# Kernel tuning notes

Measured on AMD Instinct MI355X. Metric: run time of the kernel, lower is better.

The kernel has to match this reference:

```python
import jax, jax.numpy as jnp
import numpy as np

N = 50000      # nodes
IN = 128       # in_channels
H = 2          # heads
C = 64         # hidden_channels (per head)
E = 800000     # edges (before self-loops)
OUT = 40       # out_channels
BN_EPS = 1e-5
NEG_SLOPE = 0.2  # PyG GATConv default


def _bn(x, g, b):
    # BatchNorm1d forward with batch statistics (training-mode math, biased var)
    mu = jnp.mean(x, axis=0)
    v = jnp.var(x, axis=0)
    return (x - mu) * jax.lax.rsqrt(v + BN_EPS) * g + b


def _gat_conv(x, src, dst, W, a_src, a_dst, bias, concat):
    n = x.shape[0]
    h = (x @ W).reshape(n, H, C)                      # [N,H,C] per-head projection
    al_s = jnp.einsum('nhc,hc->nh', h, a_src)         # [N,H]
    al_d = jnp.einsum('nhc,hc->nh', h, a_dst)
    e = jax.nn.leaky_relu(al_s[src] + al_d[dst], NEG_SLOPE)  # [E,H]
    # segment softmax over edges sharing the same destination
    m = jax.ops.segment_max(e, dst, num_segments=n)
    ex = jnp.exp(e - m[dst])
    s = jax.ops.segment_sum(ex, dst, num_segments=n)
    alpha = ex / s[dst]                               # [E,H]
    out = jax.ops.segment_sum(h[src] * alpha[..., None], dst, num_segments=n)  # [N,H,C]
    out = out.reshape(n, H * C) if concat else out.mean(axis=1)
    return out + bias


def setup_inputs() -> dict:
    key = jax.random.key(0)
    ks = jax.random.split(key, 16)
    g = lambda k, shp, scale=1.0: jax.random.normal(k, shp, dtype=jnp.float32) * scale
    x = g(ks[0], (N, IN))
    edge_index = jax.random.randint(ks[1], (2, E), 0, N, dtype=jnp.int32)
    s = 1.0 / np.sqrt(IN)
    s2 = 1.0 / np.sqrt(H * C)
    return {
        'x': x,
        'edge_index': edge_index,
        'bn0_g': jnp.ones((IN,), jnp.float32), 'bn0_b': jnp.zeros((IN,), jnp.float32),
        'W1': g(ks[2], (IN, H * C), s), 'a1_src': g(ks[3], (H, C), s), 'a1_dst': g(ks[4], (H, C), s),
        'b1': jnp.zeros((H * C,), jnp.float32),
        'bn1_g': jnp.ones((H * C,), jnp.float32), 'bn1_b': jnp.zeros((H * C,), jnp.float32),
        'W2': g(ks[5], (H * C, H * C), s2), 'a2_src': g(ks[6], (H, C), s2), 'a2_dst': g(ks[7], (H, C), s2),
        'b2': jnp.zeros((C,), jnp.float32),
        'bn2_g': jnp.ones((C,), jnp.float32), 'bn2_b': jnp.zeros((C,), jnp.float32),
        'Wf': g(ks[8], (C, OUT), 1.0 / np.sqrt(C)), 'bf': jnp.zeros((OUT,), jnp.float32),
    }


def reference(x, edge_index, bn0_g, bn0_b, W1, a1_src, a1_dst, b1, bn1_g, bn1_b,
              W2, a2_src, a2_dst, b2, bn2_g, bn2_b, Wf, bf):
    n = x.shape[0]
    loop = jnp.arange(n, dtype=edge_index.dtype)
    src = jnp.concatenate([edge_index[0], loop])  # add self-loops (PyG default)
    dst = jnp.concatenate([edge_index[1], loop])
    h = _bn(x, bn0_g, bn0_b)
    # layer 1: concat heads
    h = _gat_conv(h, src, dst, W1, a1_src, a1_dst, b1, concat=True)
    h = jax.nn.elu(_bn(h, bn1_g, bn1_b))
    # (dropout is identity in eval mode)
    # layer 2: average heads
    h = _gat_conv(h, src, dst, W2, a2_src, a2_dst, b2, concat=False)
    h = jax.nn.elu(_bn(h, bn2_g, bn2_b))
    return h @ Wf + bf
```

## Files before the change

kernel.cpp:

```cpp
#include <hip/hip_runtime.h>
#include <hip/hip_fp16.h>


#define NEG_SLOPE 0.2f
#define BN_EPS 1e-5f

typedef short bf16x8 __attribute__((ext_vector_type(8)));
typedef float f32x4 __attribute__((ext_vector_type(4)));

static __device__ __forceinline__ unsigned short f2bf(float f) {
    union { float f; unsigned u; } v; v.f = f;
    unsigned r = v.u + 0x7FFF + ((v.u >> 16) & 1);
    return (unsigned short)(r >> 16);
}
static __device__ __forceinline__ float2 bf2x2(unsigned v) {
    union { unsigned u; float f; } a, b;
    a.u = v << 16; b.u = v & 0xffff0000u;
    return make_float2(a.f, b.f);
}
static __device__ __forceinline__ float halfsel(unsigned p, int head) {
    __half2 h = *(__half2*)&p;
    return head ? __high2float(h) : __low2float(h);
}

__global__ void k_rank(const int* __restrict__ ei, int E, int Nn,
                       int* __restrict__ cnt, int* __restrict__ rank) {
    int i = blockIdx.x * blockDim.x + threadIdx.x;
    if (i >= E + Nn) return;
    int d = (i < E) ? ei[E + i] : (i - E);
    rank[i] = atomicAdd(&cnt[d], 1);
}

__global__ __launch_bounds__(1024) void k_part(const int* __restrict__ cnt, int Nn,
                                               int* __restrict__ part) {
    __shared__ int ws[16];
    int t = threadIdx.x, lane = t & 63, w = t >> 6;
    int i = blockIdx.x * 1024 + t;
    int v = (i < Nn) ? cnt[i] : 0;
    #pragma unroll
    for (int off = 32; off; off >>= 1) v += __shfl_xor(v, off);
    if (lane == 0) ws[w] = v;
    __syncthreads();
    if (t < 16) {
        int s = ws[t];
        #pragma unroll
        for (int off = 8; off; off >>= 1) s += __shfl_xor(s, off);
        if (t == 0) part[blockIdx.x] = s;
    }
}

__global__ __launch_bounds__(64) void k_scanp(int* __restrict__ part, int nb,
                                              int Nn, int* __restrict__ rowptr) {
    int lane = threadIdx.x;
    int carry = 0;
    for (int base = 0; base < nb; base += 64) {
        int i = base + lane;
        int v = (i < nb) ? part[i] : 0;
        int x = v;
        #pragma unroll
        for (int off = 1; off < 64; off <<= 1) {
            int y = __shfl_up(x, off);
            if (lane >= off) x += y;
        }
        if (i < nb) part[i] = carry + x - v;
        carry += __shfl(x, 63);
    }
    if (lane == 0) rowptr[Nn] = carry;
}

__global__ __launch_bounds__(1024) void k_scan2(const int* __restrict__ cnt, int Nn,
                                                const int* __restrict__ part,
                                                int* __restrict__ rowptr) {
    __shared__ int wsum[16];
    int t = threadIdx.x, lane = t & 63, w = t >> 6;
    int i = blockIdx.x * 1024 + t;
    int v = (i < Nn) ? cnt[i] : 0;
    int x = v;
    #pragma unroll
    for (int off = 1; off < 64; off <<= 1) {
        int y = __shfl_up(x, off);
        if (lane >= off) x += y;
    }
    if (lane == 63) wsum[w] = x;
    __syncthreads();
    if (w == 0) {
        int val = (lane < 16) ? wsum[lane] : 0;
        int xs = val;
        #pragma unroll
        for (int off = 1; off < 16; off <<= 1) {
            int y = __shfl_up(xs, off);
            if (lane >= off) xs += y;
        }
        if (lane < 16) wsum[lane] = xs - val;
    }
    __syncthreads();
    if (i < Nn) rowptr[i] = part[blockIdx.x] + wsum[w] + (x - v);
}

__global__ void k_fill2(const int* __restrict__ ei, const int* __restrict__ rank,
                        const int* __restrict__ rowptr, int E, int Nn,
                        int* __restrict__ ssrc) {
    int i = blockIdx.x * blockDim.x + threadIdx.x;
    if (i >= E + Nn) return;
    int s, d;
    if (i < E) { s = ei[i]; d = ei[E + i]; }
    else       { s = i - E; d = s; }
    ssrc[rowptr[d] + rank[i]] = s;
}

template <int C>
__global__ __launch_bounds__(256) void k_bnstat2(const float* __restrict__ x, int M,
                                                 int rowsPerBlock, float* __restrict__ sums) {
    constexpr int TPR = C / 4;
    constexpr int RS  = 256 / TPR;
    __shared__ float red[4][2 * C];
    const int t = threadIdx.x;
    const int cg = t % TPR, rg = t / TPR, w = t >> 6, lane = t & 63;
    int r0 = blockIdx.x * rowsPerBlock + rg;
    int r1 = min(M, blockIdx.x * rowsPerBlock + rowsPerBlock);
    float4 s = make_float4(0, 0, 0, 0), q = make_float4(0, 0, 0, 0);
    #pragma unroll 4
    for (int r = r0; r < r1; r += RS) {
        float4 v = *(const float4*)&x[(size_t)r * C + cg * 4];
        s.x += v.x; s.y += v.y; s.z += v.z; s.w += v.w;
        q.x += v.x * v.x; q.y += v.y * v.y; q.z += v.z * v.z; q.w += v.w * v.w;
    }
    #pragma unroll
    for (int off = TPR; off < 64; off <<= 1) {
        s.x += __shfl_xor(s.x, off); s.y += __shfl_xor(s.y, off);
        s.z += __shfl_xor(s.z, off); s.w += __shfl_xor(s.w, off);
        q.x += __shfl_xor(q.x, off); q.y += __shfl_xor(q.y, off);
        q.z += __shfl_xor(q.z, off); q.w += __shfl_xor(q.w, off);
    }
    if (lane < TPR) {
        *(float4*)&red[w][cg * 4] = s;
        *(float4*)&red[w][C + cg * 4] = q;
    }
    __syncthreads();
    for (int idx = t; idx < 2 * C; idx += 256) {
        float tot = red[0][idx] + red[1][idx] + red[2][idx] + red[3][idx];
        atomicAdd(&sums[idx], tot);
    }
}

__global__ void k_bnfin(const float* __restrict__ sums, int M, int C,
                        const float* __restrict__ g, const float* __restrict__ b,
                        float* __restrict__ st) {
    int c = threadIdx.x;
    if (c < C) {
        float mu = sums[c] / (float)M;
        float var = sums[C + c] / (float)M - mu * mu;
        float s = g[c] * rsqrtf(var + BN_EPS);
        st[c] = s;
        st[C + c] = b[c] - mu * s;
    }
}

__global__ __launch_bounds__(256) void k_wt2(const float* __restrict__ W1, const float* __restrict__ W2,
                                             unsigned short* __restrict__ wt1, unsigned short* __restrict__ wt2) {
    int idx = blockIdx.x * 256 + threadIdx.x;
    if (idx >= 128 * 128) return;
    int n = idx >> 7, k = idx & 127;
    wt1[idx] = f2bf(W1[k * 128 + n]);
    wt2[idx] = f2bf(W2[k * 128 + n]);
}

__global__ __launch_bounds__(256) void k_mfma(
    const float* __restrict__ A, const unsigned short* __restrict__ wt,
    const float* __restrict__ stp, int elu,
    const float* __restrict__ asrc, const float* __restrict__ adst, int M,
    unsigned short* __restrict__ hb, float* __restrict__ als, float* __restrict__ ald) {
    __shared__ unsigned short As[64 * 136];
    __shared__ unsigned short Bs[128 * 136];
    const int t = threadIdx.x;
    const int w = t >> 6, lane = t & 63;
    const int c = lane & 15, q = lane >> 4;
    const int row0 = blockIdx.x * 64;

    #pragma unroll
    for (int i = 0; i < 8; i++) {
        int idx = t + i * 256;
        int r = idx >> 5, ch4 = idx & 31;
        int gr = row0 + r;
        float4 v = make_float4(0, 0, 0, 0);
        if (gr < M) {
            v = *(const float4*)&A[(size_t)gr * 128 + ch4 * 4];
            float4 sc = *(const float4*)&stp[ch4 * 4];
            float4 sh = *(const float4*)&stp[128 + ch4 * 4];
            v.x = v.x * sc.x + sh.x; v.y = v.y * sc.y + sh.y;
            v.z = v.z * sc.z + sh.z; v.w = v.w * sc.w + sh.w;
            if (elu) {
                v.x = v.x > 0.f ? v.x : expm1f(v.x);
                v.y = v.y > 0.f ? v.y : expm1f(v.y);
                v.z = v.z > 0.f ? v.z : expm1f(v.z);
                v.w = v.w > 0.f ? v.w : expm1f(v.w);
            }
        }
        unsigned p0 = ((unsigned)f2bf(v.y) << 16) | f2bf(v.x);
        unsigned p1 = ((unsigned)f2bf(v.w) << 16) | f2bf(v.z);
        *(uint2*)&As[r * 136 + ch4 * 4] = make_uint2(p0, p1);
    }
    #pragma unroll
    for (int i = 0; i < 8; i++) {
        int idx = t + i * 256;
        int r = idx >> 4, ch = idx & 15;
        *(uint4*)&Bs[r * 136 + ch * 8] = *(const uint4*)&wt[(size_t)r * 128 + ch * 8];
    }
    __syncthreads();

    f32x4 acc[8] = {};
    #pragma unroll
    for (int ks = 0; ks < 4; ks++) {
        bf16x8 a = *(bf16x8*)&As[(w * 16 + c) * 136 + (ks * 4 + q) * 8];
        #pragma unroll
        for (int tl = 0; tl < 8; tl++) {
            bf16x8 b = *(bf16x8*)&Bs[(tl * 16 + c) * 136 + (ks * 4 + q) * 8];
            acc[tl] = __builtin_amdgcn_mfma_f32_16x16x32_bf16(a, b, acc[tl], 0, 0, 0);
        }
    }

    #pragma unroll
    for (int reg = 0; reg < 4; reg++) {
        int grow = row0 + w * 16 + q * 4 + reg;
        if (grow < M) {
            #pragma unroll
            for (int tl = 0; tl < 8; tl++)
                hb[(size_t)grow * 128 + tl * 16 + c] = f2bf(acc[tl][reg]);
        }
    }

    float as_[8], ad_[8];
    #pragma unroll
    for (int tl = 0; tl < 8; tl++) { as_[tl] = asrc[tl * 16 + c]; ad_[tl] = adst[tl * 16 + c]; }
    #pragma unroll
    for (int reg = 0; reg < 4; reg++) {
        float s0 = 0.f, s1 = 0.f, d0 = 0.f, d1 = 0.f;
        #pragma unroll
        for (int tl = 0; tl < 4; tl++) { s0 += acc[tl][reg] * as_[tl]; d0 += acc[tl][reg] * ad_[tl]; }
        #pragma unroll
        for (int tl = 4; tl < 8; tl++) { s1 += acc[tl][reg] * as_[tl]; d1 += acc[tl][reg] * ad_[tl]; }
        #pragma unroll
        for (int off = 1; off < 16; off <<= 1) {
            s0 += __shfl_xor(s0, off); s1 += __shfl_xor(s1, off);
            d0 += __shfl_xor(d0, off); d1 += __shfl_xor(d1, off);
        }
        int grow = row0 + w * 16 + q * 4 + reg;
        if (c == 0 && grow < M) {
            *(float2*)&als[(size_t)grow * 2] = make_float2(s0, s1);
            *(float2*)&ald[(size_t)grow * 2] = make_float2(d0, d1);
        }
    }
}

static __device__ __forceinline__ void acc8(float* acc, uint4 v, float a) {
    float2 p;
    p = bf2x2(v.x); acc[0] += a * p.x; acc[1] += a * p.y;
    p = bf2x2(v.y); acc[2] += a * p.x; acc[3] += a * p.y;
    p = bf2x2(v.z); acc[4] += a * p.x; acc[5] += a * p.y;
    p = bf2x2(v.w); acc[6] += a * p.x; acc[7] += a * p.y;
}

template <int MEAN>
static __device__ __forceinline__ void attnagg(
    const int* __restrict__ rowptr, const int* __restrict__ ssrc,
    const float* __restrict__ als, const float* __restrict__ ald,
    float* __restrict__ alpha, const unsigned short* __restrict__ hb,
    const float* __restrict__ bias, int Nn, float* __restrict__ out) {
    int gw = (blockIdx.x * blockDim.x + threadIdx.x) >> 6;
    if (gw >= Nn) return;
    int lane = threadIdx.x & 63;
    int sub = lane >> 4, c = lane & 15, head = c >> 3;
    int beg = rowptr[gw], end = rowptr[gw + 1];
    int deg = end - beg;
    float2 dv = *(const float2*)&ald[(size_t)gw * 2];
    float acc[8] = {};

    if (deg <= 64) {
        bool on = lane < deg;
        int eidx = beg + (on ? lane : 0);
        int sreg = ssrc[eidx];
        float2 av = *(const float2*)&als[(size_t)sreg * 2];
        float v0 = av.x + dv.x; v0 = v0 > 0.f ? v0 : NEG_SLOPE * v0;
        float v1 = av.y + dv.y; v1 = v1 > 0.f ? v1 : NEG_SLOPE * v1;
        float m0 = on ? v0 : -1e30f, m1 = on ? v1 : -1e30f;
        #pragma unroll
        for (int off = 32; off; off >>= 1) {
            m0 = fmaxf(m0, __shfl_xor(m0, off));
            m1 = fmaxf(m1, __shfl_xor(m1, off));
        }
        float p0 = on ? __expf(v0 - m0) : 0.f;
        float p1 = on ? __expf(v1 - m1) : 0.f;
        float t0 = p0, t1 = p1;
        #pragma unroll
        for (int off = 32; off; off >>= 1) {
            t0 += __shfl_xor(t0, off);
            t1 += __shfl_xor(t1, off);
        }
        __half2 hpk = __floats2half2_rn(p0 / t0, p1 / t1);
        int pk = *(int*)&hpk;

        int nit = (deg + 3) >> 2;
        for (int it = 0; it < nit; it += 2) {
            int j0 = it * 4 + sub;
            int j1 = j0 + 4;
            int sa = __shfl(sreg, j0 & 63);
            int sb = __shfl(sreg, j1 & 63);
            unsigned pa = (unsigned)__shfl(pk, j0 & 63);
            unsigned pb = (unsigned)__shfl(pk, j1 & 63);
            float aa = halfsel(pa, head);
            float ab = halfsel(pb, head);
            if (j0 < deg) {
                uint4 va = *(const uint4*)&hb[(size_t)sa * 128 + c * 8];
                acc8(acc, va, aa);
            }
            if (j1 < deg) {
                uint4 vb = *(const uint4*)&hb[(size_t)sb * 128 + c * 8];
                acc8(acc, vb, ab);
            }
        }
    } else {
        float d0 = dv.x, d1 = dv.y;
        float m0 = -1e30f, m1 = -1e30f;
        for (int e = beg + lane; e < end; e += 64) {
            int s = ssrc[e];
            float v0 = als[s * 2] + d0;     v0 = v0 > 0.f ? v0 : NEG_SLOPE * v0;
            float v1 = als[s * 2 + 1] + d1; v1 = v1 > 0.f ? v1 : NEG_SLOPE * v1;
            m0 = fmaxf(m0, v0); m1 = fmaxf(m1, v1);
        }
        #pragma unroll
        for (int off = 32; off; off >>= 1) {
            m0 = fmaxf(m0, __shfl_xor(m0, off));
            m1 = fmaxf(m1, __shfl_xor(m1, off));
        }
        float t0 = 0.f, t1 = 0.f;
        for (int e = beg + lane; e < end; e += 64) {
            int s = ssrc[e];
            float v0 = als[s * 2] + d0;     v0 = v0 > 0.f ? v0 : NEG_SLOPE * v0;
            float v1 = als[s * 2 + 1] + d1; v1 = v1 > 0.f ? v1 : NEG_SLOPE * v1;
            float p0 = __expf(v0 - m0), p1 = __expf(v1 - m1);
            alpha[e * 2] = p0; alpha[e * 2 + 1] = p1;
            t0 += p0; t1 += p1;
        }
        #pragma unroll
        for (int off = 32; off; off >>= 1) {
            t0 += __shfl_xor(t0, off);
            t1 += __shfl_xor(t1, off);
        }
        float i0 = 1.f / t0, i1 = 1.f / t1;
        for (int e = beg + sub; e < end; e += 4) {
            int s = ssrc[e];
            float a = (head ? alpha[(size_t)e * 2 + 1] * i1 : alpha[(size_t)e * 2] * i0);
            uint4 v = *(const uint4*)&hb[(size_t)s * 128 + c * 8];
            acc8(acc, v, a);
        }
    }

    #pragma unroll
    for (int j2 = 0; j2 < 8; j2++) {
        acc[j2] += __shfl_xor(acc[j2], 16);
        acc[j2] += __shfl_xor(acc[j2], 32);
        if (MEAN) acc[j2] += __shfl_xor(acc[j2], 8);
    }
    if (MEAN) {
        if (sub == 0 && c < 8) {
            float4 b0 = *(const float4*)&bias[c * 8];
            float4 b1 = *(const float4*)&bias[c * 8 + 4];
            float4 o0 = make_float4(0.5f * acc[0] + b0.x, 0.5f * acc[1] + b0.y, 0.5f * acc[2] + b0.z, 0.5f * acc[3] + b0.w);
            float4 o1 = make_float4(0.5f * acc[4] + b1.x, 0.5f * acc[5] + b1.y, 0.5f * acc[6] + b1.z, 0.5f * acc[7] + b1.w);
            *(float4*)&out[(size_t)gw * 64 + c * 8] = o0;
            *(float4*)&out[(size_t)gw * 64 + c * 8 + 4] = o1;
        }
    } else {
        if (sub == 0) {
            float4 b0 = *(const float4*)&bias[c * 8];
            float4 b1 = *(const float4*)&bias[c * 8 + 4];
            float4 o0 = make_float4(acc[0] + b0.x, acc[1] + b0.y, acc[2] + b0.z, acc[3] + b0.w);
            float4 o1 = make_float4(acc[4] + b1.x, acc[5] + b1.y, acc[6] + b1.z, acc[7] + b1.w);
            *(float4*)&out[(size_t)gw * 128 + c * 8] = o0;
            *(float4*)&out[(size_t)gw * 128 + c * 8 + 4] = o1;
        }
    }
}

__global__ __launch_bounds__(256) void k_attnagg1(const int* __restrict__ rowptr, const int* __restrict__ ssrc,
                                                  const float* __restrict__ als, const float* __restrict__ ald,
                                                  float* __restrict__ alpha, const unsigned short* __restrict__ hb,
                                                  const float* __restrict__ bias, int Nn, float* __restrict__ out) {
    attnagg<0>(rowptr, ssrc, als, ald, alpha, hb, bias, Nn, out);
}

__global__ __launch_bounds__(256) void k_attnagg2(const int* __restrict__ rowptr, const int* __restrict__ ssrc,
                                                  const float* __restrict__ als, const float* __restrict__ ald,
                                                  float* __restrict__ alpha, const unsigned short* __restrict__ hb,
                                                  const float* __restrict__ bias, int Nn, float* __restrict__ out) {
    attnagg<1>(rowptr, ssrc, als, ald, alpha, hb, bias, Nn, out);
}

__global__ __launch_bounds__(128) void k_gemmf(const float* __restrict__ A, const float* __restrict__ Wf,
                                               const float* __restrict__ bf, const float* __restrict__ st,
                                               int M, float* __restrict__ out) {
    __shared__ float As[128 * 65];
    __shared__ float Bs[64 * 40];
    int t = threadIdx.x;
    int row0 = blockIdx.x * 128;
    for (int i = t; i < 64 * 40; i += 128) Bs[i] = Wf[i];
    for (int i = t; i < 128 * 64; i += 128) {
        int r = i >> 6, k = i & 63;
        int gr = row0 + r;
        float v = 0.f;
        if (gr < M) {
            v = A[(size_t)gr * 64 + k] * st[k] + st[64 + k];
            v = v > 0.f ? v : expm1f(v);
        }
        As[r * 65 + k] = v;
    }
    __syncthreads();
    int cg = t & 3, rg = t >> 2;
    float acc[4][10] = {};
    for (int k = 0; k < 64; k++) {
        float b[10];
        #pragma unroll
        for (int j = 0; j < 10; j++) b[j] = Bs[k * 40 + cg * 10 + j];
        #pragma unroll
        for (int r = 0; r < 4; r++) {
            float a = As[(rg * 4 + r) * 65 + k];
            #pragma unroll
            for (int j = 0; j < 10; j++) acc[r][j] += a * b[j];
        }
    }
    for (int r = 0; r < 4; r++) {
        int gr = row0 + rg * 4 + r;
        if (gr < M) {
            #pragma unroll
            for (int j = 0; j < 10; j++) out[(size_t)gr * 40 + cg * 10 + j] = acc[r][j] + bf[cg * 10 + j];
        }
    }
}

extern "C" void kernel_launch(void* const* d_in, const int* in_sizes, int n_in,
                              void* d_out, int out_size, void* d_ws, size_t ws_size,
                              hipStream_t stream) {
    const float* x     = (const float*)d_in[0];
    const int*   ei    = (const int*)d_in[1];
    const float* bn0_g = (const float*)d_in[2];
    const float* bn0_b = (const float*)d_in[3];
    const float* W1    = (const float*)d_in[4];
    const float* a1s   = (const float*)d_in[5];
    const float* a1d   = (const float*)d_in[6];
    const float* b1    = (const float*)d_in[7];
    const float* bn1_g = (const float*)d_in[8];
    const float* bn1_b = (const float*)d_in[9];
    const float* W2    = (const float*)d_in[10];
    const float* a2s   = (const float*)d_in[11];
    const float* a2d   = (const float*)d_in[12];
    const float* b2    = (const float*)d_in[13];
    const float* bn2_g = (const float*)d_in[14];
    const float* bn2_b = (const float*)d_in[15];
    const float* Wf    = (const float*)d_in[16];
    const float* bf    = (const float*)d_in[17];
    float* out = (float*)d_out;

    const int N  = in_sizes[0] / 128;
    const int E  = in_sizes[1] / 2;
    const int ET = E + N;

    char* ws = (char*)d_ws;
    size_t off = 0;
    auto alloc = [&](size_t bytes) -> char* {
        char* p = ws + off;
        off = (off + bytes + 255) & ~(size_t)255;
        return p;
    };
    int*   cnt    = (int*)alloc((size_t)N * 4);
    int*   rowptr = (int*)alloc((size_t)(N + 1) * 4);
    int*   ssrc   = (int*)alloc((size_t)ET * 4);
    float* abuf   = (float*)alloc((size_t)N * 128 * 4);
    unsigned short* hb  = (unsigned short*)alloc((size_t)N * 128 * 2);
    unsigned short* wt1 = (unsigned short*)alloc((size_t)128 * 128 * 2);
    unsigned short* wt2 = (unsigned short*)alloc((size_t)128 * 128 * 2);
    float* alpha  = (float*)alloc((size_t)ET * 2 * 4);
    float* als    = (float*)alloc((size_t)N * 2 * 4);
    float* ald    = (float*)alloc((size_t)N * 2 * 4);
    int*   part   = (int*)alloc(1024 * 4);
    float* sums   = (float*)alloc(640 * 4);
    float* st     = (float*)alloc(256 * 4);
    int*   rank   = (int*)hb;

    const int tb = 256;
    const int egrid = (ET + tb - 1) / tb;
    const int wgrid = ((size_t)N * 64 + tb - 1) / tb;
    const int ggrid = (N + 63) / 64;
    const int nscan = (N + 1023) / 1024;
    const int bgrid = (N + 255) / 256;

    hipMemsetAsync(cnt, 0, (size_t)N * 4, stream);
    hipMemsetAsync(sums, 0, 640 * 4, stream);
    k_rank<<<egrid, tb, 0, stream>>>(ei, E, N, cnt, rank);
    k_part<<<nscan, 1024, 0, stream>>>(cnt, N, part);
    k_scanp<<<1, 64, 0, stream>>>(part, nscan, N, rowptr);
    k_scan2<<<nscan, 1024, 0, stream>>>(cnt, N, part, rowptr);
    k_fill2<<<egrid, tb, 0, stream>>>(ei, rank, rowptr, E, N, ssrc);

    k_wt2<<<64, tb, 0, stream>>>(W1, W2, wt1, wt2);

    k_bnstat2<128><<<bgrid, 256, 0, stream>>>(x, N, 256, sums);
    k_bnfin<<<1, 128, 0, stream>>>(sums, N, 128, bn0_g, bn0_b, st);

    k_mfma<<<ggrid, tb, 0, stream>>>(x, wt1, st, 0, a1s, a1d, N, hb, als, ald);
    k_attnagg1<<<wgrid, tb, 0, stream>>>(rowptr, ssrc, als, ald, alpha, hb, b1, N, abuf);

    k_bnstat2<128><<<bgrid, 256, 0, stream>>>(abuf, N, 256, sums + 256);
    k_bnfin<<<1, 128, 0, stream>>>(sums + 256, N, 128, bn1_g, bn1_b, st);

    k_mfma<<<ggrid, tb, 0, stream>>>(abuf, wt2, st, 1, a2s, a2d, N, hb, als, ald);
    k_attnagg2<<<wgrid, tb, 0, stream>>>(rowptr, ssrc, als, ald, alpha, hb, b2, N, abuf);

    k_bnstat2<64><<<bgrid, 256, 0, stream>>>(abuf, N, 256, sums + 512);
    k_bnfin<<<1, 64, 0, stream>>>(sums + 512, N, 64, bn2_g, bn2_b, st);

    k_gemmf<<<(N + 127) / 128, 128, 0, stream>>>(abuf, Wf, bf, st, N, out);
}
```

Measured before the change: 340.4 us.

## Fuse small setup kernels, use last-block BN finalize, unroll gather loop

Result: slower. 365.3 us (+7.3%).

```diff
diff --git a/kernel.cpp b/kernel.cpp
--- a/kernel.cpp
+++ b/kernel.cpp
@@ -23,12 +23,23 @@
     return head ? __high2float(h) : __low2float(h);
 }
 
-__global__ void k_rank(const int* __restrict__ ei, int E, int Nn,
-                       int* __restrict__ cnt, int* __restrict__ rank) {
+__global__ void k_rankwt(const int* __restrict__ ei, int E, int Nn, int egrid,
+                         int* __restrict__ cnt, unsigned short* __restrict__ rank,
+                         const float* __restrict__ W1, const float* __restrict__ W2,
+                         unsigned short* __restrict__ wt1, unsigned short* __restrict__ wt2) {
+    if (blockIdx.x >= egrid) {
+        int idx = (blockIdx.x - egrid) * 256 + threadIdx.x;
+        if (idx < 128 * 128) {
+            int n = idx >> 7, k = idx & 127;
+            wt1[idx] = f2bf(W1[k * 128 + n]);
+            wt2[idx] = f2bf(W2[k * 128 + n]);
+        }
+        return;
+    }
     int i = blockIdx.x * blockDim.x + threadIdx.x;
     if (i >= E + Nn) return;
     int d = (i < E) ? ei[E + i] : (i - E);
-    rank[i] = atomicAdd(&cnt[d], 1);
+    rank[i] = (unsigned short)atomicAdd(&cnt[d], 1);
 }
 
 __global__ __launch_bounds__(1024) void k_part(const int* __restrict__ cnt, int Nn,
@@ -49,31 +60,29 @@
     }
 }
 
-__global__ __launch_bounds__(64) void k_scanp(int* __restrict__ part, int nb,
-                                              int Nn, int* __restrict__ rowptr) {
-    int lane = threadIdx.x;
-    int carry = 0;
-    for (int base = 0; base < nb; base += 64) {
-        int i = base + lane;
-        int v = (i < nb) ? part[i] : 0;
-        int x = v;
-        #pragma unroll
-        for (int off = 1; off < 64; off <<= 1) {
-            int y = __shfl_up(x, off);
-            if (lane >= off) x += y;
-        }
-        if (i < nb) part[i] = carry + x - v;
-        carry += __shfl(x, 63);
-    }
-    if (lane == 0) rowptr[Nn] = carry;
-}
-
-__global__ __launch_bounds__(1024) void k_scan2(const int* __restrict__ cnt, int Nn,
+__global__ __launch_bounds__(1024) void k_scan2(const int* __restrict__ cnt, int Nn, int nb,
                                                 const int* __restrict__ part,
                                                 int* __restrict__ rowptr) {
     __shared__ int wsum[16];
+    __shared__ int s_base, s_total;
     int t = threadIdx.x, lane = t & 63, w = t >> 6;
-    int i = blockIdx.x * 1024 + t;
+    int b = blockIdx.x;
+    if (w == 0) {
+        int base = 0, total = 0;
+        for (int ch = 0; ch < nb; ch += 64) {
+            int j = ch + lane;
+            int v = (j < nb) ? part[j] : 0;
+            total += v;
+            base += (j < b) ? v : 0;
+        }
+        #pragma unroll
+        for (int off = 32; off; off >>= 1) {
+            base += __shfl_xor(base, off);
+            total += __shfl_xor(total, off);
+        }
+        if (lane == 0) { s_base = base; s_total = total; }
+    }
+    int i = b * 1024 + t;
     int v = (i < Nn) ? cnt[i] : 0;
     int x = v;
     #pragma unroll
@@ -94,10 +103,11 @@
         if (lane < 16) wsum[lane] = xs - val;
     }
     __syncthreads();
-    if (i < Nn) rowptr[i] = part[blockIdx.x] + wsum[w] + (x - v);
-}
-
-__global__ void k_fill2(const int* __restrict__ ei, const int* __restrict__ rank,
+    if (i < Nn) rowptr[i] = s_base + wsum[w] + (x - v);
+    if (b == gridDim.x - 1 && t == 0) rowptr[Nn] = s_total;
+}
+
+__global__ void k_fill2(const int* __restrict__ ei, const unsigned short* __restrict__ rank,
                         const int* __restrict__ rowptr, int E, int Nn,
                         int* __restrict__ ssrc) {
     int i = blockIdx.x * blockDim.x + threadIdx.x;
@@ -105,15 +115,18 @@
     int s, d;
     if (i < E) { s = ei[i]; d = ei[E + i]; }
     else       { s = i - E; d = s; }
-    ssrc[rowptr[d] + rank[i]] = s;
+    ssrc[rowptr[d] + (int)rank[i]] = s;
 }
 
 template <int C>
 __global__ __launch_bounds__(256) void k_bnstat2(const float* __restrict__ x, int M,
-                                                 int rowsPerBlock, float* __restrict__ sums) {
+                                                 int rowsPerBlock, float* __restrict__ sums,
+                                                 const float* __restrict__ g, const float* __restrict__ b,
+                                                 float* __restrict__ st, int* __restrict__ ticket) {
     constexpr int TPR = C / 4;
     constexpr int RS  = 256 / TPR;
     __shared__ float red[4][2 * C];
+    __shared__ int lastFlag;
     const int t = threadIdx.x;
     const int cg = t % TPR, rg = t / TPR, w = t >> 6, lane = t & 63;
     int r0 = blockIdx.x * rowsPerBlock + rg;
@@ -141,28 +154,21 @@
         float tot = red[0][idx] + red[1][idx] + red[2][idx] + red[3][idx];
         atomicAdd(&sums[idx], tot);
     }
-}
-
-__global__ void k_bnfin(const float* __restrict__ sums, int M, int C,
-                        const float* __restrict__ g, const float* __restrict__ b,
-                        float* __restrict__ st) {
-    int c = threadIdx.x;
-    if (c < C) {
-        float mu = sums[c] / (float)M;
-        float var = sums[C + c] / (float)M - mu * mu;
-        float s = g[c] * rsqrtf(var + BN_EPS);
-        st[c] = s;
-        st[C + c] = b[c] - mu * s;
-    }
-}
-
-__global__ __launch_bounds__(256) void k_wt2(const float* __restrict__ W1, const float* __restrict__ W2,
-                                             unsigned short* __restrict__ wt1, unsigned short* __restrict__ wt2) {
-    int idx = blockIdx.x * 256 + threadIdx.x;
-    if (idx >= 128 * 128) return;
-    int n = idx >> 7, k = idx & 127;
-    wt1[idx] = f2bf(W1[k * 128 + n]);
-    wt2[idx] = f2bf(W2[k * 128 + n]);
+    __threadfence();
+    if (t == 0) {
+        int old = __hip_atomic_fetch_add(ticket, 1, __ATOMIC_ACQ_REL, __HIP_MEMORY_SCOPE_AGENT);
+        lastFlag = (old == (int)gridDim.x - 1);
+    }
+    __syncthreads();
+    if (lastFlag && t < C) {
+        float ss = __hip_atomic_load(&sums[t], __ATOMIC_RELAXED, __HIP_MEMORY_SCOPE_AGENT);
+        float qq = __hip_atomic_load(&sums[C + t], __ATOMIC_RELAXED, __HIP_MEMORY_SCOPE_AGENT);
+        float mu = ss / (float)M;
+        float var = qq / (float)M - mu * mu;
+        float sc = g[t] * rsqrtf(var + BN_EPS);
+        st[t] = sc;
+        st[C + t] = b[t] - mu * sc;
+    }
 }
 
 __global__ __launch_bounds__(256) void k_mfma(
@@ -300,22 +306,21 @@
         int pk = *(int*)&hpk;
 
         int nit = (deg + 3) >> 2;
-        for (int it = 0; it < nit; it += 2) {
-            int j0 = it * 4 + sub;
-            int j1 = j0 + 4;
-            int sa = __shfl(sreg, j0 & 63);
-            int sb = __shfl(sreg, j1 & 63);
-            unsigned pa = (unsigned)__shfl(pk, j0 & 63);
-            unsigned pb = (unsigned)__shfl(pk, j1 & 63);
-            float aa = halfsel(pa, head);
-            float ab = halfsel(pb, head);
-            if (j0 < deg) {
-                uint4 va = *(const uint4*)&hb[(size_t)sa * 128 + c * 8];
-                acc8(acc, va, aa);
+        for (int it = 0; it < nit; it += 4) {
+            int jj[4], s_[4]; unsigned p_[4];
+            #pragma unroll
+            for (int u = 0; u < 4; u++) {
+                jj[u] = (it + u) * 4 + sub;
+                int ls = jj[u] & 63;
+                s_[u] = __shfl(sreg, ls);
+                p_[u] = (unsigned)__shfl(pk, ls);
             }
-            if (j1 < deg) {
-                uint4 vb = *(const uint4*)&hb[(size_t)sb * 128 + c * 8];
-                acc8(acc, vb, ab);
+            #pragma unroll
+            for (int u = 0; u < 4; u++) {
+                if (jj[u] < deg) {
+                    uint4 v = *(const uint4*)&hb[(size_t)s_[u] * 128 + c * 8];
+                    acc8(acc, v, halfsel(p_[u], head));
+                }
             }
         }
     } else {
@@ -482,9 +487,10 @@
     float* als    = (float*)alloc((size_t)N * 2 * 4);
     float* ald    = (float*)alloc((size_t)N * 2 * 4);
     int*   part   = (int*)alloc(1024 * 4);
-    float* sums   = (float*)alloc(640 * 4);
+    float* sums   = (float*)alloc(768 * 4);
     float* st     = (float*)alloc(256 * 4);
-    int*   rank   = (int*)hb;
+    unsigned short* rank = (unsigned short*)hb;
+    int* tickets = (int*)(sums + 640);
 
     const int tb = 256;
     const int egrid = (ET + tb - 1) / tb;
@@ -494,29 +500,23 @@
     const int bgrid = (N + 255) / 256;
 
     hipMemsetAsync(cnt, 0, (size_t)N * 4, stream);
-    hipMemsetAsync(sums, 0, 640 * 4, stream);
-    k_rank<<<egrid, tb, 0, stream>>>(ei, E, N, cnt, rank);
+    hipMemsetAsync(sums, 0, 768 * 4, stream);
+    k_rankwt<<<egrid + 64, tb, 0, stream>>>(ei, E, N, egrid, cnt, rank, W1, W2, wt1, wt2);
     k_part<<<nscan, 1024, 0, stream>>>(cnt, N, part);
-    k_scanp<<<1, 64, 0, stream>>>(part, nscan, N, rowptr);
-    k_scan2<<<nscan, 1024, 0, stream>>>(cnt, N, part, rowptr);
+    k_scan2<<<nscan, 1024, 0, stream>>>(cnt, N, nscan, part, rowptr);
     k_fill2<<<egrid, tb, 0, stream>>>(ei, rank, rowptr, E, N, ssrc);
 
-    k_wt2<<<64, tb, 0, stream>>>(W1, W2, wt1, wt2);
-
-    k_bnstat2<128><<<bgrid, 256, 0, stream>>>(x, N, 256, sums);
-    k_bnfin<<<1, 128, 0, stream>>>(sums, N, 128, bn0_g, bn0_b, st);
+    k_bnstat2<128><<<bgrid, 256, 0, stream>>>(x, N, 256, sums, bn0_g, bn0_b, st, tickets);
 
     k_mfma<<<ggrid, tb, 0, stream>>>(x, wt1, st, 0, a1s, a1d, N, hb, als, ald);
     k_attnagg1<<<wgrid, tb, 0, stream>>>(rowptr, ssrc, als, ald, alpha, hb, b1, N, abuf);
 
-    k_bnstat2<128><<<bgrid, 256, 0, stream>>>(abuf, N, 256, sums + 256);
-    k_bnfin<<<1, 128, 0, stream>>>(sums + 256, N, 128, bn1_g, bn1_b, st);
+    k_bnstat2<128><<<bgrid, 256, 0, stream>>>(abuf, N, 256, sums + 256, bn1_g, bn1_b, st, tickets + 1);
 
     k_mfma<<<ggrid, tb, 0, stream>>>(abuf, wt2, st, 1, a2s, a2d, N, hb, als, ald);
     k_attnagg2<<<wgrid, tb, 0, stream>>>(rowptr, ssrc, als, ald, alpha, hb, b2, N, abuf);
 
-    k_bnstat2<64><<<bgrid, 256, 0, stream>>>(abuf, N, 256, sums + 512);
-    k_bnfin<<<1, 64, 0, stream>>>(sums + 512, N, 64, bn2_g, bn2_b, st);
+    k_bnstat2<64><<<bgrid, 256, 0, stream>>>(abuf, N, 256, sums + 512, bn2_g, bn2_b, st, tickets + 2);
 
     k_gemmf<<<(N + 127) / 128, 128, 0, stream>>>(abuf, Wf, bf, st, N, out);
 }
```
